# Performance work log

Measured on AMD Instinct MI355X. Metric: run time of the kernel, lower is better.

The kernel has to match this reference:

```python
import jax, jax.numpy as jnp
import numpy as np
import math

B, S, H = 2, 2048, 4096
NH, HD, KVH = 32, 128, 8
GROUPS = NH // KVH  # repeat_kv n_rep
BASE = 10000.0
TRAINING_SEQLEN = 8192
BASE_SEQLEN = 8192


def _rope_cos_sin(s):
    # RotaryEmbedding.forward: seq_len = max(s, training_seqlen); NTK-alpha scaled base; mscale
    seq_len = max(s, TRAINING_SEQLEN)
    context_value = math.log(seq_len / BASE_SEQLEN, 2) + 1
    ntk_alpha = max(2 ** math.ceil(context_value) - 1, 1)
    scale = seq_len / TRAINING_SEQLEN
    mscale = 1.0 if scale <= 1 else 0.1 * math.log(scale) + 1.0
    base = BASE * ntk_alpha ** (HD / (HD - 2))
    inv_freq = 1.0 / base ** (np.arange(0, HD, 2, dtype=np.float32) / HD)
    t = np.arange(seq_len, dtype=np.float32)
    freqs = np.outer(t, inv_freq)          # [seq_len, HD/2]
    emb = np.concatenate([freqs, freqs], axis=-1)  # [seq_len, HD]
    return jnp.asarray(mscale * np.cos(emb)[:s]), jnp.asarray(mscale * np.sin(emb)[:s])


def _rotate_half(x):
    x1, x2 = jnp.split(x, 2, axis=-1)
    return jnp.concatenate([-x2, x1], axis=-1)


def setup_inputs() -> dict:
    key = jax.random.key(0)
    ks = jax.random.split(key, 5)
    hidden_states = jax.random.normal(ks[0], (B, S, H), jnp.float32)
    residual = jax.random.normal(ks[1], (B, S, H), jnp.float32)
    causal = jnp.triu(jnp.ones((S, S), dtype=bool), k=1)  # True = masked (masked_fill semantics)
    attention_mask = jnp.broadcast_to(causal[None, None], (B, 1, S, S))
    W_q = jax.random.normal(ks[2], (H, H), jnp.float32) / np.float32(np.sqrt(H))
    W_kv = jax.random.normal(ks[3], (H, 2 * KVH * HD), jnp.float32) / np.float32(np.sqrt(H))
    W_dense = jax.random.normal(ks[4], (H, H), jnp.float32) / np.float32(np.sqrt(H))
    b_dense = jnp.zeros((H,), jnp.float32)
    return dict(hidden_states=hidden_states, residual=residual, attention_mask=attention_mask,
                W_q=W_q, W_kv=W_kv, W_dense=W_dense, b_dense=b_dense)


def reference(hidden_states, residual, attention_mask, W_q, W_kv, W_dense, b_dense):
    # QKV projections (Linear, no bias for query/key_value)
    q = (hidden_states @ W_q).reshape(B, S, NH, HD)            # [B,S,NH,HD]
    kvp = (hidden_states @ W_kv).reshape(B, S, KVH, 2 * HD)
    k, v = kvp[..., :HD], kvp[..., HD:]                        # [B,S,KVH,HD]
    # rotary (NTK-scaled), applied identically to q and k
    cos, sin = _rope_cos_sin(S)
    cos = cos[None, :, None, :]
    sin = sin[None, :, None, :]
    q = q * cos + _rotate_half(q) * sin
    k = k * cos + _rotate_half(k) * sin
    # repeat_kv: each kv head repeated GROUPS times consecutively
    k = jnp.repeat(k, GROUPS, axis=2)                          # [B,S,NH,HD]
    v = jnp.repeat(v, GROUPS, axis=2)
    # scaled dot-product attention with causal mask
    scores = jnp.einsum('bqhd,bkhd->bhqk', q, k) * (1.0 / np.float32(np.sqrt(HD)))
    scores = jnp.where(attention_mask, jnp.finfo(scores.dtype).min, scores)
    probs = jax.nn.softmax(scores, axis=-1)                    # attention_dropout=0 (eval)
    ctx = jnp.einsum('bhqk,bkhd->bqhd', probs, v).reshape(B, S, H)
    # dense (with bias) + dropout_add residual (dropout inactive in eval)
    out = ctx @ W_dense + b_dense
    return residual + out
```

## Files before the change

kernel.cpp:

```cpp
#include <hip/hip_runtime.h>
#include <hip/hip_bf16.h>


#define BB   2
#define SS   2048
#define HH   4096
#define NHH  32
#define HDD  128
#define KVHH 8

typedef unsigned short u16;
typedef __attribute__((ext_vector_type(8))) short  short8;
typedef __attribute__((ext_vector_type(4))) float  floatx4;

#define AS1 __attribute__((address_space(1)))
#define AS3 __attribute__((address_space(3)))

__device__ __forceinline__ void gll16(const void* g, void* l) {
    __builtin_amdgcn_global_load_lds((const AS1 unsigned int*)g,
                                     (AS3 unsigned int*)l, 16, 0, 0);
}
__device__ __forceinline__ float b2f(u16 x) {
    union { unsigned int u; float f; } c; c.u = ((unsigned int)x) << 16; return c.f;
}
__device__ __forceinline__ u16 f2b(float f) {
    union { float f; unsigned int u; } c; c.f = f;
    unsigned int r = 0x7FFFu + ((c.u >> 16) & 1u);
    return (u16)((c.u + r) >> 16);
}

__global__ __launch_bounds__(256)
void cvt_kernel(const float* __restrict__ X, u16* __restrict__ Y, int n4) {
    int i = blockIdx.x * 256 + threadIdx.x;
    if (i >= n4) return;
    float4 v = *(const float4*)(X + (size_t)i * 4);
    size_t o = (size_t)i * 4;
    Y[o + 0] = f2b(v.x); Y[o + 1] = f2b(v.y);
    Y[o + 2] = f2b(v.z); Y[o + 3] = f2b(v.w);
}

__global__ __launch_bounds__(256) void rope_table(float* __restrict__ ct,
                                                  float* __restrict__ st) {
    int idx = blockIdx.x * 256 + threadIdx.x;
    if (idx >= SS * 64) return;
    int s = idx >> 6, i = idx & 63;
    double inv = pow(10000.0, -(double)(2 * i) / 128.0);
    double f = (double)s * inv;
    ct[idx] = (float)cos(f);
    st[idx] = (float)sin(f);
}

__global__ __launch_bounds__(256) void wt_kernel(const float* __restrict__ W,
                                                 u16* __restrict__ WT,
                                                 int R, int C) {
    __shared__ u16 t[64 * 65];
    int tcols = C >> 6;
    int ty = blockIdx.x / tcols, tx = blockIdx.x % tcols;
    int r0 = ty * 64, c0 = tx * 64;
    for (int idx = threadIdx.x; idx < 4096; idx += 256) {
        int r = idx >> 6, c = idx & 63;
        t[r * 65 + c] = f2b(W[(size_t)(r0 + r) * C + c0 + c]);
    }
    __syncthreads();
    for (int idx = threadIdx.x; idx < 4096; idx += 256) {
        int c = idx >> 6, r = idx & 63;
        WT[(size_t)(c0 + c) * R + r0 + r] = t[r * 65 + c];
    }
}

__global__ __launch_bounds__(256, 2)
void gemm_bt(const u16* __restrict__ A, const u16* __restrict__ BT,
             u16* __restrict__ C, float* __restrict__ Cf,
             int M, int N, int K,
             const float* __restrict__ bias, const float* __restrict__ resid) {
    __shared__ u16 sA[128 * 32];
    __shared__ u16 sB[128 * 32];
    const int tid = threadIdx.x;
    const int wave = tid >> 6, lane = tid & 63;
    const int m0 = blockIdx.y * 128, n0 = blockIdx.x * 128;
    const int wm = (wave >> 1) * 64, wn = (wave & 1) * 64;
    const int srow = lane >> 2, scol = (lane & 3) * 8;
    const int frow = lane & 15, fquad = lane >> 4;
    const int fk = fquad * 8;

    const floatx4 fz = {0.f, 0.f, 0.f, 0.f};
    floatx4 acc[4][4];
#pragma unroll
    for (int i = 0; i < 4; ++i)
#pragma unroll
        for (int j = 0; j < 4; ++j) acc[i][j] = fz;

    for (int kt = 0; kt < K; kt += 32) {
#pragma unroll
        for (int j = 0; j < 2; ++j) {
            int rb = (wave + j * 4) * 16;
            gll16(A  + (size_t)(m0 + rb + srow) * K + kt + scol, &sA[rb * 32]);
            gll16(BT + (size_t)(n0 + rb + srow) * K + kt + scol, &sB[rb * 32]);
        }
        __syncthreads();
        short8 af[4];
#pragma unroll
        for (int i = 0; i < 4; ++i)
            af[i] = *(const short8*)&sA[(wm + i * 16 + frow) * 32 + fk];
#pragma unroll
        for (int jn = 0; jn < 4; ++jn) {
            short8 bfr = *(const short8*)&sB[(wn + jn * 16 + frow) * 32 + fk];
#pragma unroll
            for (int i = 0; i < 4; ++i)
                acc[i][jn] = __builtin_amdgcn_mfma_f32_16x16x32_bf16(
                    af[i], bfr, acc[i][jn], 0, 0, 0);
        }
        __syncthreads();
    }
#pragma unroll
    for (int i = 0; i < 4; ++i) {
#pragma unroll
        for (int jn = 0; jn < 4; ++jn) {
            int col = n0 + wn + jn * 16 + frow;
            float bv = bias ? bias[col] : 0.f;
#pragma unroll
            for (int r = 0; r < 4; ++r) {
                int row = m0 + wm + i * 16 + fquad * 4 + r;
                float v = acc[i][jn][r] + bv;
                if (Cf) {
                    if (resid) v += resid[(size_t)row * N + col];
                    Cf[(size_t)row * N + col] = v;
                } else {
                    C[(size_t)row * N + col] = f2b(v);
                }
            }
        }
    }
}

__global__ __launch_bounds__(256)
void rope_apply(u16* __restrict__ Qb, u16* __restrict__ KVb,
                const float* __restrict__ ct, const float* __restrict__ st) {
    int gid = blockIdx.x * 256 + threadIdx.x;
    int row = gid >> 6, d = gid & 63;
    const int nq = BB * SS * NHH;
    u16* p;
    int s;
    if (row < nq) {
        s = (row / NHH) % SS;
        p = Qb + (size_t)row * HDD;
    } else {
        int r2 = row - nq;
        s = (r2 / KVHH) % SS;
        p = KVb + (size_t)r2 * 256;
    }
    float c = ct[s * 64 + d], sn = st[s * 64 + d];
    float x0 = b2f(p[d]), x1 = b2f(p[d + 64]);
    p[d]      = f2b(x0 * c - x1 * sn);
    p[d + 64] = f2b(x1 * c + x0 * sn);
}

__global__ __launch_bounds__(256)
void vt_kernel(const u16* __restrict__ KVb, u16* __restrict__ VT) {
    __shared__ u16 t[64 * 130];
    int bid = blockIdx.x;
    int bk = bid >> 5;
    int s0 = (bid & 31) * 64;
    int b = bk >> 3, kvh = bk & 7;
    for (int idx = threadIdx.x; idx < 64 * 128; idx += 256) {
        int si = idx >> 7, d = idx & 127;
        t[si * 130 + d] =
            KVb[((size_t)((b * SS + s0 + si) * KVHH + kvh)) * 256 + 128 + d];
    }
    __syncthreads();
    for (int idx = threadIdx.x; idx < 64 * 128; idx += 256) {
        int d = idx >> 6, sj = idx & 63;
        VT[((size_t)(bk * HDD + d)) * SS + s0 + sj] = t[sj * 130 + d];
    }
}

__global__ __launch_bounds__(256, 2)
void attn(const u16* __restrict__ Q, const u16* __restrict__ KV,
          const u16* __restrict__ VT, u16* __restrict__ CTX) {
    __shared__ u16 sK[64 * 128];
    __shared__ u16 sVT[128 * 64];
    __shared__ u16 sQP[128 * 128];

    const int tid = threadIdx.x;
    const int wave = tid >> 6, lane = tid & 63;
    const int frow = lane & 15, fquad = lane >> 4;
    const int bid = blockIdx.x;
    const int h = bid & 31;
    const int qt = (bid >> 5) & 15;
    const int b = bid >> 9;
    const int kvh = h >> 2;
    const int q0 = qt * 128;

    {
        const int srow4 = lane >> 4, scol16 = (lane & 15) * 8;
#pragma unroll
        for (int j = 0; j < 8; ++j) {
            int rb = (j * 4 + wave) * 4;
            gll16(Q + ((size_t)((b * SS + q0 + rb + srow4) * NHH + h)) * HDD + scol16,
                  &sQP[rb * 128]);
        }
    }
    __syncthreads();
    short8 qf[2][4];
#pragma unroll
    for (int mi = 0; mi < 2; ++mi)
#pragma unroll
        for (int ds = 0; ds < 4; ++ds)
            qf[mi][ds] = *(const short8*)
                &sQP[(wave * 32 + mi * 16 + frow) * 128 + ds * 32 + fquad * 8];

    const floatx4 fz = {0.f, 0.f, 0.f, 0.f};
    floatx4 o[2][8];
#pragma unroll
    for (int mi = 0; mi < 2; ++mi)
#pragma unroll
        for (int dn = 0; dn < 8; ++dn) o[mi][dn] = fz;
    float mrow[2][4], lrow[2][4];
#pragma unroll
    for (int mi = 0; mi < 2; ++mi)
#pragma unroll
        for (int r = 0; r < 4; ++r) { mrow[mi][r] = -1e30f; lrow[mi][r] = 0.f; }

    const float scale = 0.08838834764831845f;
    const int nt = 2 * (qt + 1);
    for (int t = 0; t < nt; ++t) {
        const int k0 = t * 64;
        {
            int srow4 = lane >> 4, scol16 = (lane & 15) * 8;
#pragma unroll
            for (int j = 0; j < 4; ++j) {
                int rb = (j * 4 + wave) * 4;
                gll16(KV + ((size_t)((b * SS + k0 + rb + srow4) * KVHH + kvh)) * 256 + scol16,
                      &sK[rb * 128]);
            }
            int srow8 = lane >> 3, scol8 = (lane & 7) * 8;
#pragma unroll
            for (int j = 0; j < 4; ++j) {
                int rb = (j * 4 + wave) * 8;
                gll16(VT + ((size_t)((b * KVHH + kvh) * HDD + rb + srow8)) * SS + k0 + scol8,
                      &sVT[rb * 64]);
            }
        }
        __syncthreads();

        floatx4 sc[2][4];
#pragma unroll
        for (int mi = 0; mi < 2; ++mi)
#pragma unroll
            for (int ni = 0; ni < 4; ++ni) sc[mi][ni] = fz;
#pragma unroll
        for (int ds = 0; ds < 4; ++ds) {
#pragma unroll
            for (int ni = 0; ni < 4; ++ni) {
                short8 kf = *(const short8*)
                    &sK[(ni * 16 + frow) * 128 + ds * 32 + fquad * 8];
                sc[0][ni] = __builtin_amdgcn_mfma_f32_16x16x32_bf16(
                    qf[0][ds], kf, sc[0][ni], 0, 0, 0);
                sc[1][ni] = __builtin_amdgcn_mfma_f32_16x16x32_bf16(
                    qf[1][ds], kf, sc[1][ni], 0, 0, 0);
            }
        }

        const bool dgt = (t >= 2 * qt);
#pragma unroll
        for (int mi = 0; mi < 2; ++mi) {
#pragma unroll
            for (int r = 0; r < 4; ++r) {
                int qg = q0 + wave * 32 + mi * 16 + fquad * 4 + r;
                float mx = -1e30f;
#pragma unroll
                for (int ni = 0; ni < 4; ++ni) {
                    float v = sc[mi][ni][r] * scale;
                    if (dgt) {
                        int kg = k0 + ni * 16 + frow;
                        if (kg > qg) v = -1e30f;
                    }
                    sc[mi][ni][r] = v;
                    mx = fmaxf(mx, v);
                }
                mx = fmaxf(mx, __shfl_xor(mx, 1));
                mx = fmaxf(mx, __shfl_xor(mx, 2));
                mx = fmaxf(mx, __shfl_xor(mx, 4));
                mx = fmaxf(mx, __shfl_xor(mx, 8));
                float mold = mrow[mi][r];
                float mnew = fmaxf(mold, mx);
                float alpha = __expf(mold - mnew);
                mrow[mi][r] = mnew;
                float rs = 0.f;
#pragma unroll
                for (int ni = 0; ni < 4; ++ni) {
                    float pv = __expf(sc[mi][ni][r] - mnew);
                    sc[mi][ni][r] = pv;
                    rs += pv;
                }
                rs += __shfl_xor(rs, 1);
                rs += __shfl_xor(rs, 2);
                rs += __shfl_xor(rs, 4);
                rs += __shfl_xor(rs, 8);
                lrow[mi][r] = lrow[mi][r] * alpha + rs;
#pragma unroll
                for (int dn = 0; dn < 8; ++dn) o[mi][dn][r] *= alpha;
            }
        }

#pragma unroll
        for (int mi = 0; mi < 2; ++mi)
#pragma unroll
            for (int ni = 0; ni < 4; ++ni)
#pragma unroll
                for (int r = 0; r < 4; ++r)
                    sQP[(wave * 32 + mi * 16 + fquad * 4 + r) * 72 + ni * 16 + frow] =
                        f2b(sc[mi][ni][r]);
        __syncthreads();

#pragma unroll
        for (int ks = 0; ks < 2; ++ks) {
            short8 pf0 = *(const short8*)
                &sQP[(wave * 32 + frow) * 72 + ks * 32 + fquad * 8];
            short8 pf1 = *(const short8*)
                &sQP[(wave * 32 + 16 + frow) * 72 + ks * 32 + fquad * 8];
#pragma unroll
            for (int dn = 0; dn < 8; ++dn) {
                short8 vf = *(const short8*)
                    &sVT[(dn * 16 + frow) * 64 + ks * 32 + fquad * 8];
                o[0][dn] = __builtin_amdgcn_mfma_f32_16x16x32_bf16(pf0, vf, o[0][dn], 0, 0, 0);
                o[1][dn] = __builtin_amdgcn_mfma_f32_16x16x32_bf16(pf1, vf, o[1][dn], 0, 0, 0);
            }
        }
        __syncthreads();
    }

#pragma unroll
    for (int mi = 0; mi < 2; ++mi) {
#pragma unroll
        for (int r = 0; r < 4; ++r) {
            float inv = 1.f / lrow[mi][r];
            int qg = q0 + wave * 32 + mi * 16 + fquad * 4 + r;
            size_t base = ((size_t)(b * SS + qg) * NHH + h) * HDD;
#pragma unroll
            for (int dn = 0; dn < 8; ++dn)
                CTX[base + dn * 16 + frow] = f2b(o[mi][dn][r] * inv);
        }
    }
}

extern "C" void kernel_launch(void* const* d_in, const int* in_sizes, int n_in,
                              void* d_out, int out_size, void* d_ws, size_t ws_size,
                              hipStream_t stream) {
    const float* hidden = (const float*)d_in[0];
    const float* resid  = (const float*)d_in[1];
    const float* Wq  = (const float*)d_in[3];
    const float* Wkv = (const float*)d_in[4];
    const float* Wd  = (const float*)d_in[5];
    const float* bd  = (const float*)d_in[6];
    float* out = (float*)d_out;

    char* ws = (char*)d_ws;
    u16*   hsb = (u16*)(ws);
    u16*   Qb  = (u16*)(ws + ((size_t)32 << 20));
    u16*   KVb = (u16*)(ws + ((size_t)64 << 20));
    u16*   T1  = (u16*)(ws + ((size_t)80 << 20));
    u16*   VTb = (u16*)(ws + ((size_t)112 << 20));
    float* ct  = (float*)(ws + ((size_t)120 << 20));
    float* st  = (float*)(ws + ((size_t)120 << 20) + ((size_t)512 << 10));

    const int M = BB * SS;

    rope_table<<<512, 256, 0, stream>>>(ct, st);
    cvt_kernel<<<(M * HH / 4 + 255) / 256, 256, 0, stream>>>(hidden, hsb, M * HH / 4);

    wt_kernel<<<4096, 256, 0, stream>>>(Wq, T1, HH, HH);
    gemm_bt<<<dim3(32, 32), 256, 0, stream>>>(hsb, T1, Qb, nullptr, M, HH, HH,
                                              nullptr, nullptr);
    wt_kernel<<<2048, 256, 0, stream>>>(Wkv, T1, HH, 2 * KVHH * HDD);
    gemm_bt<<<dim3(16, 32), 256, 0, stream>>>(hsb, T1, KVb, nullptr,
                                              M, 2 * KVHH * HDD, HH,
                                              nullptr, nullptr);

    rope_apply<<<(BB * SS * (NHH + KVHH) * 64) / 256, 256, 0, stream>>>(Qb, KVb, ct, st);
    vt_kernel<<<BB * KVHH * (SS / 64), 256, 0, stream>>>(KVb, VTb);

    attn<<<BB * 16 * NHH, 256, 0, stream>>>(Qb, KVb, VTb, Qb);

    wt_kernel<<<4096, 256, 0, stream>>>(Wd, T1, HH, HH);
    gemm_bt<<<dim3(32, 32), 256, 0, stream>>>(Qb, T1, nullptr, out, M, HH, HH,
                                              bd, resid);
}
```

Baseline: 1.031 ms.

## Swizzle attention LDS tiles, shrink shared memory, reorder blocks heavy-first

The attention kernel now applies an XOR swizzle to the K, V^T and Q tiles in LDS so fragment reads avoid bank conflicts. Q is staged through the same buffer that later holds K and V, which cuts shared memory so three blocks can be resident per CU instead of two. Blocks are remapped so the longest causal query tiles are scheduled first, and the block barrier before the P·V step is replaced by a wave-local lgkmcnt wait, since each wave reads only its own rows of P. Risks are higher register pressure under the tighter launch bound and relying on wave-private P rows being correct without the barrier.

```diff
diff --git a/kernel.cpp b/kernel.cpp
--- a/kernel.cpp
+++ b/kernel.cpp
@@ -174,30 +174,33 @@
     }
 }
 
-__global__ __launch_bounds__(256, 2)
+__global__ __launch_bounds__(256, 3)
 void attn(const u16* __restrict__ Q, const u16* __restrict__ KV,
           const u16* __restrict__ VT, u16* __restrict__ CTX) {
-    __shared__ u16 sK[64 * 128];
-    __shared__ u16 sVT[128 * 64];
-    __shared__ u16 sQP[128 * 128];
+    __shared__ u16 smem[25600];
+    u16* sK  = smem;
+    u16* sVT = smem + 8192;
+    u16* sP  = smem + 16384;
 
     const int tid = threadIdx.x;
     const int wave = tid >> 6, lane = tid & 63;
     const int frow = lane & 15, fquad = lane >> 4;
     const int bid = blockIdx.x;
+    const int qt = 15 - (bid >> 6);
+    const int b = (bid >> 5) & 1;
     const int h = bid & 31;
-    const int qt = (bid >> 5) & 15;
-    const int b = bid >> 9;
     const int kvh = h >> 2;
     const int q0 = qt * 128;
 
     {
-        const int srow4 = lane >> 4, scol16 = (lane & 15) * 8;
+        const int srow4 = lane >> 4;
+        const int chunk = lane & 15;
 #pragma unroll
         for (int j = 0; j < 8; ++j) {
             int rb = (j * 4 + wave) * 4;
-            gll16(Q + ((size_t)((b * SS + q0 + rb + srow4) * NHH + h)) * HDD + scol16,
-                  &sQP[rb * 128]);
+            int sc = chunk ^ ((rb + srow4) & 7);
+            gll16(Q + ((size_t)((b * SS + q0 + rb + srow4) * NHH + h)) * HDD + sc * 8,
+                  &smem[rb * 128]);
         }
     }
     __syncthreads();
@@ -207,7 +210,9 @@
 #pragma unroll
         for (int ds = 0; ds < 4; ++ds)
             qf[mi][ds] = *(const short8*)
-                &sQP[(wave * 32 + mi * 16 + frow) * 128 + ds * 32 + fquad * 8];
+                &smem[(wave * 32 + mi * 16 + frow) * 128 +
+                      ((ds * 4 + fquad) ^ (frow & 7)) * 8];
+    __syncthreads();
 
     const floatx4 fz = {0.f, 0.f, 0.f, 0.f};
     floatx4 o[2][8];
@@ -226,18 +231,20 @@
     for (int t = 0; t < nt; ++t) {
         const int k0 = t * 64;
         {
-            int srow4 = lane >> 4, scol16 = (lane & 15) * 8;
+            const int srow4 = lane >> 4, ch16 = lane & 15;
 #pragma unroll
             for (int j = 0; j < 4; ++j) {
                 int rb = (j * 4 + wave) * 4;
-                gll16(KV + ((size_t)((b * SS + k0 + rb + srow4) * KVHH + kvh)) * 256 + scol16,
+                int sc = ch16 ^ ((rb + srow4) & 7);
+                gll16(KV + ((size_t)((b * SS + k0 + rb + srow4) * KVHH + kvh)) * 256 + sc * 8,
                       &sK[rb * 128]);
             }
-            int srow8 = lane >> 3, scol8 = (lane & 7) * 8;
+            const int srow8 = lane >> 3, ch8 = lane & 7;
 #pragma unroll
             for (int j = 0; j < 4; ++j) {
                 int rb = (j * 4 + wave) * 8;
-                gll16(VT + ((size_t)((b * KVHH + kvh) * HDD + rb + srow8)) * SS + k0 + scol8,
+                int sc = ch8 ^ ((rb + srow8) & 7);
+                gll16(VT + ((size_t)((b * KVHH + kvh) * HDD + rb + srow8)) * SS + k0 + sc * 8,
                       &sVT[rb * 64]);
             }
         }
@@ -253,7 +260,8 @@
 #pragma unroll
             for (int ni = 0; ni < 4; ++ni) {
                 short8 kf = *(const short8*)
-                    &sK[(ni * 16 + frow) * 128 + ds * 32 + fquad * 8];
+                    &sK[(ni * 16 + frow) * 128 +
+                        ((ds * 4 + fquad) ^ (frow & 7)) * 8];
                 sc[0][ni] = __builtin_amdgcn_mfma_f32_16x16x32_bf16(
                     qf[0][ds], kf, sc[0][ni], 0, 0, 0);
                 sc[1][ni] = __builtin_amdgcn_mfma_f32_16x16x32_bf16(
@@ -309,20 +317,21 @@
             for (int ni = 0; ni < 4; ++ni)
 #pragma unroll
                 for (int r = 0; r < 4; ++r)
-                    sQP[(wave * 32 + mi * 16 + fquad * 4 + r) * 72 + ni * 16 + frow] =
+                    sP[(wave * 32 + mi * 16 + fquad * 4 + r) * 72 + ni * 16 + frow] =
                         f2b(sc[mi][ni][r]);
-        __syncthreads();
+        asm volatile("s_waitcnt lgkmcnt(0)" ::: "memory");
 
 #pragma unroll
         for (int ks = 0; ks < 2; ++ks) {
             short8 pf0 = *(const short8*)
-                &sQP[(wave * 32 + frow) * 72 + ks * 32 + fquad * 8];
+                &sP[(wave * 32 + frow) * 72 + ks * 32 + fquad * 8];
             short8 pf1 = *(const short8*)
-                &sQP[(wave * 32 + 16 + frow) * 72 + ks * 32 + fquad * 8];
+                &sP[(wave * 32 + 16 + frow) * 72 + ks * 32 + fquad * 8];
 #pragma unroll
             for (int dn = 0; dn < 8; ++dn) {
                 short8 vf = *(const short8*)
-                    &sVT[(dn * 16 + frow) * 64 + ks * 32 + fquad * 8];
+                    &sVT[(dn * 16 + frow) * 64 +
+                         ((ks * 4 + fquad) ^ (frow & 7)) * 8];
                 o[0][dn] = __builtin_amdgcn_mfma_f32_16x16x32_bf16(pf0, vf, o[0][dn], 0, 0, 0);
                 o[1][dn] = __builtin_amdgcn_mfma_f32_16x16x32_bf16(pf1, vf, o[1][dn], 0, 0, 0);
             }
```

After: 1.004 ms. 2.6% less time.
